# Performance work log

Hardware: AMD Instinct MI355X
Metric: run time of the kernel (lower is better)

## Reference

```python
import jax, jax.numpy as jnp
import numpy as np

N_NODES = 100000
N_EDGES = 3200000
D_NODE = 32
D_EDGE = 6


def _mlp2(x, W1, b1, W2, b2):
    # Linear -> ReLU -> Linear -> ReLU
    h = jax.nn.relu(x @ W1 + b1)
    return jax.nn.relu(h @ W2 + b2)


def setup_inputs() -> dict:
    key = jax.random.key(0)
    ks = jax.random.split(key, 12)
    glorot = lambda k, fi, fo: jax.random.normal(k, (fi, fo), jnp.float32) * (2.0 / (fi + fo)) ** 0.5
    return {
        "x_node": jax.random.normal(ks[0], (N_NODES, D_NODE), jnp.float32),
        "x_edge": jax.random.normal(ks[1], (N_EDGES, D_EDGE), jnp.float32),
        "src": jax.random.randint(ks[2], (N_EDGES,), 0, N_NODES, jnp.int32),
        "dst": jax.random.randint(ks[3], (N_EDGES,), 0, N_NODES, jnp.int32),
        # edge_msg_encoder: 70 -> 32 -> 6
        "We1": glorot(ks[4], 70, 32), "be1": jnp.zeros((32,), jnp.float32),
        "We2": glorot(ks[5], 32, 6), "be2": jnp.zeros((6,), jnp.float32),
        # node_msg_encoder: 38 -> 64 -> 32
        "Wn1": glorot(ks[6], 38, 64), "bn1": jnp.zeros((64,), jnp.float32),
        "Wn2": glorot(ks[7], 64, 32), "bn2": jnp.zeros((32,), jnp.float32),
    }


def reference(x_node, x_edge, src, dst, We1, be1, We2, be2, Wn1, bn1, Wn2, bn2):
    # Gather endpoint node features per edge
    x_dst = x_node[dst]                                   # [E, 32]
    x_src = x_node[src]                                   # [E, 32]
    edge_in = jnp.concatenate([x_dst, x_src, x_edge], 1)  # [E, 70]
    edge_msg = _mlp2(edge_in, We1, be1, We2, be2)         # [E, 6]
    node_in = jnp.concatenate([x_dst, edge_msg], 1)       # [E, 38]
    node_msg = _mlp2(node_in, Wn1, bn1, Wn2, bn2)         # [E, 32]
    # reduce_udf: sum of incoming messages per destination node
    nm = jax.ops.segment_sum(node_msg, dst, num_segments=N_NODES)  # [N, 32]
    return nm, edge_msg
```

## Files before the change

### kernel.cpp

```cpp
#include <hip/hip_runtime.h>

#define N_EDGES 3200000
#define N_NODES 100000

typedef unsigned short ushort_t;
typedef __attribute__((ext_vector_type(8))) short bf16x8;
typedef __attribute__((ext_vector_type(4))) float f32x4;

__device__ inline unsigned short f2bf(float f) {
    unsigned u = __float_as_uint(f);
    u += 0x7fffu + ((u >> 16) & 1u);
    return (unsigned short)(u >> 16);
}
__device__ inline unsigned pack_bf2(float lo, float hi) {
    return (unsigned)f2bf(lo) | ((unsigned)f2bf(hi) << 16);
}
__device__ inline float bflo(unsigned u) { return __uint_as_float(u << 16); }
__device__ inline float bfhi(unsigned u) { return __uint_as_float(u & 0xffff0000u); }
__device__ inline bf16x8 u4_to_b8(uint4 u) {
    union { uint4 a; bf16x8 b; } c; c.a = u; return c.b;
}

__global__ void __launch_bounds__(256) mpn_precompute(
    const float* __restrict__ x_node,
    const float* __restrict__ We1, const float* __restrict__ be1,
    const float* __restrict__ We2, const float* __restrict__ be2,
    const float* __restrict__ Wn1, const float* __restrict__ bn1,
    const float* __restrict__ Wn2,
    unsigned* __restrict__ xb,
    ushort_t* __restrict__ WaT, ushort_t* __restrict__ WbT,
    ushort_t* __restrict__ WcTp, ushort_t* __restrict__ W2T,
    ushort_t* __restrict__ NaT, ushort_t* __restrict__ NbTp,
    ushort_t* __restrict__ N2T, float* __restrict__ be2p,
    float* __restrict__ nm_out)
{
    const int n = blockIdx.x * 256 + threadIdx.x;

    if (n < 1024) {
        const int o = n >> 5, k = n & 31;
        WaT[n] = f2bf(We1[k * 32 + o]);
        WbT[n] = f2bf(We1[(32 + k) * 32 + o]);
        WcTp[n] = (k < 6) ? f2bf(We1[(64 + k) * 32 + o])
                          : ((k == 6) ? f2bf(be1[o]) : (ushort_t)0);
    }
    if (n < 512) {
        const int o = n >> 5, k = n & 31;
        W2T[n] = (o < 6) ? f2bf(We2[k * 6 + o]) : (ushort_t)0;
    }
    if (n < 2048) {
        const int o = n >> 5, k = n & 31;
        NaT[n] = f2bf(Wn1[k * 64 + o]);
        NbTp[n] = (k < 6) ? f2bf(Wn1[(32 + k) * 64 + o])
                          : ((k == 6) ? f2bf(bn1[o]) : (ushort_t)0);
        N2T[n] = f2bf(Wn2[(n & 63) * 32 + (n >> 6)]);
    }
    if (n < 16) be2p[n] = (n < 6) ? be2[n] : 0.0f;

    if (n >= N_NODES) return;

    {
        float4 z = make_float4(0.f, 0.f, 0.f, 0.f);
        float4* o = (float4*)(nm_out + (size_t)n * 32);
        #pragma unroll
        for (int i = 0; i < 8; ++i) o[i] = z;
    }
    {
        const float4* px = (const float4*)(x_node + (size_t)n * 32);
        unsigned* xr = xb + (size_t)n * 16;
        #pragma unroll
        for (int i = 0; i < 8; ++i) {
            float4 v = px[i];
            xr[2*i+0] = pack_bf2(v.x, v.y);
            xr[2*i+1] = pack_bf2(v.z, v.w);
        }
    }
}

__global__ void __launch_bounds__(256, 4) mpn_main(
    const ushort_t* __restrict__ xb,
    const ushort_t* __restrict__ WaT, const ushort_t* __restrict__ WbT,
    const ushort_t* __restrict__ WcTp, const ushort_t* __restrict__ W2T,
    const ushort_t* __restrict__ NaT, const ushort_t* __restrict__ NbTp,
    const ushort_t* __restrict__ N2T,
    const float* __restrict__ be2p, const float* __restrict__ bn2,
    const float* __restrict__ x_edge,
    const int* __restrict__ src, const int* __restrict__ dst,
    float* __restrict__ nm_out,
    float* __restrict__ em_out)
{
    __shared__ unsigned s_nmb[128 * 17];
    __shared__ int s_d[128];

    const int tid  = threadIdx.x;
    const int lane = tid & 63;
    const int wave = tid >> 6;
    const int q    = (lane >> 4) & 3;
    const int l15  = lane & 15;
    const int hi   = q >> 1;

    const int eb = blockIdx.x * 128 + wave * 32;

    int dv[2], sv[2];
    #pragma unroll
    for (int t = 0; t < 2; ++t) {
        const int e = eb + t * 16 + l15;
        dv[t] = dst[e];
        sv[t] = src[e];
    }
    bf16x8 xd[2], xs[2];
    #pragma unroll
    for (int t = 0; t < 2; ++t) {
        xd[t] = *(const bf16x8*)(xb + (size_t)dv[t] * 32 + q * 8);
        xs[t] = *(const bf16x8*)(xb + (size_t)sv[t] * 32 + q * 8);
    }
    uint4 bxeU[2];
    #pragma unroll
    for (int t = 0; t < 2; ++t) {
        uint4 u = make_uint4(0, 0, 0, 0);
        if (q == 0) {
            const int e = eb + t * 16 + l15;
            const float2* pe = (const float2*)(x_edge + (size_t)e * 6);
            float2 a = pe[0], b = pe[1], c = pe[2];
            u = make_uint4(pack_bf2(a.x, a.y), pack_bf2(b.x, b.y),
                           pack_bf2(c.x, c.y), pack_bf2(1.0f, 0.0f));
        }
        bxeU[t] = u;
    }

    const int sAl = ((q & 1) << 5) + l15;
    const int sBl = sAl + 16;

    #pragma unroll
    for (int t = 0; t < 2; ++t) {
        f32x4 h1c[2];
        #pragma unroll
        for (int m = 0; m < 2; ++m) {
            const int row = m * 16 + l15;
            f32x4 acc = (f32x4)0.f;
            acc = __builtin_amdgcn_mfma_f32_16x16x32_bf16(
                *(const bf16x8*)(WaT + row * 32 + q * 8), xd[t], acc, 0, 0, 0);
            acc = __builtin_amdgcn_mfma_f32_16x16x32_bf16(
                *(const bf16x8*)(WbT + row * 32 + q * 8), xs[t], acc, 0, 0, 0);
            acc = __builtin_amdgcn_mfma_f32_16x16x32_bf16(
                *(const bf16x8*)(WcTp + row * 32 + q * 8), u4_to_b8(bxeU[t]), acc, 0, 0, 0);
            #pragma unroll
            for (int r = 0; r < 4; ++r) acc[r] = fmaxf(acc[r], 0.f);
            h1c[m] = acc;
        }

        unsigned u00 = pack_bf2(h1c[0][0], h1c[0][1]);
        unsigned u01 = pack_bf2(h1c[0][2], h1c[0][3]);
        unsigned u10 = pack_bf2(h1c[1][0], h1c[1][1]);
        unsigned u11 = pack_bf2(h1c[1][2], h1c[1][3]);
        unsigned a0 = __shfl((int)u00, sAl), a1 = __shfl((int)u01, sAl);
        unsigned a2 = __shfl((int)u10, sAl), a3 = __shfl((int)u11, sAl);
        unsigned b0 = __shfl((int)u00, sBl), b1 = __shfl((int)u01, sBl);
        unsigned b2 = __shfl((int)u10, sBl), b3 = __shfl((int)u11, sBl);
        uint4 bh1 = make_uint4(hi ? a2 : a0, hi ? a3 : a1,
                               hi ? b2 : b0, hi ? b3 : b1);

        f32x4 emc = __builtin_amdgcn_mfma_f32_16x16x32_bf16(
            *(const bf16x8*)(W2T + l15 * 32 + q * 8), u4_to_b8(bh1),
            (f32x4)0.f, 0, 0, 0);
        const float emv0 = fmaxf(emc[0] + be2p[q * 4 + 0], 0.f);
        const float emv1 = fmaxf(emc[1] + be2p[q * 4 + 1], 0.f);
        const float emv2 = fmaxf(emc[2] + be2p[q * 4 + 2], 0.f);
        const float emv3 = fmaxf(emc[3] + be2p[q * 4 + 3], 0.f);

        const int e = eb + t * 16 + l15;
        if (q == 0) {
            *(float2*)(em_out + (size_t)e * 6 + 0) = make_float2(emv0, emv1);
            *(float2*)(em_out + (size_t)e * 6 + 2) = make_float2(emv2, emv3);
        } else if (q == 1) {
            *(float2*)(em_out + (size_t)e * 6 + 4) = make_float2(emv0, emv1);
        }

        const float f4 = __shfl(emv0, l15 + 16);
        const float f5 = __shfl(emv1, l15 + 16);
        uint4 bem = make_uint4(0, 0, 0, 0);
        if (q == 0)
            bem = make_uint4(pack_bf2(emv0, emv1), pack_bf2(emv2, emv3),
                             pack_bf2(f4, f5), pack_bf2(1.0f, 0.0f));

        f32x4 h2c[4];
        #pragma unroll
        for (int m = 0; m < 4; ++m) {
            const int row = m * 16 + l15;
            f32x4 acc = __builtin_amdgcn_mfma_f32_16x16x32_bf16(
                *(const bf16x8*)(NbTp + row * 32 + q * 8), u4_to_b8(bem),
                (f32x4)0.f, 0, 0, 0);
            acc = __builtin_amdgcn_mfma_f32_16x16x32_bf16(
                *(const bf16x8*)(NaT + row * 32 + q * 8), xd[t], acc, 0, 0, 0);
            #pragma unroll
            for (int r = 0; r < 4; ++r) acc[r] = fmaxf(acc[r], 0.f);
            h2c[m] = acc;
        }

        unsigned v00 = pack_bf2(h2c[0][0], h2c[0][1]), v01 = pack_bf2(h2c[0][2], h2c[0][3]);
        unsigned v10 = pack_bf2(h2c[1][0], h2c[1][1]), v11 = pack_bf2(h2c[1][2], h2c[1][3]);
        unsigned v20 = pack_bf2(h2c[2][0], h2c[2][1]), v21 = pack_bf2(h2c[2][2], h2c[2][3]);
        unsigned v30 = pack_bf2(h2c[3][0], h2c[3][1]), v31 = pack_bf2(h2c[3][2], h2c[3][3]);
        unsigned c0 = __shfl((int)v00, sAl), c1 = __shfl((int)v01, sAl);
        unsigned c2 = __shfl((int)v10, sAl), c3 = __shfl((int)v11, sAl);
        unsigned d0 = __shfl((int)v00, sBl), d1 = __shfl((int)v01, sBl);
        unsigned d2 = __shfl((int)v10, sBl), d3 = __shfl((int)v11, sBl);
        uint4 bh2k0 = make_uint4(hi ? c2 : c0, hi ? c3 : c1,
                                 hi ? d2 : d0, hi ? d3 : d1);
        unsigned g0 = __shfl((int)v20, sAl), g1 = __shfl((int)v21, sAl);
        unsigned g2 = __shfl((int)v30, sAl), g3 = __shfl((int)v31, sAl);
        unsigned k0 = __shfl((int)v20, sBl), k1 = __shfl((int)v21, sBl);
        unsigned k2 = __shfl((int)v30, sBl), k3 = __shfl((int)v31, sBl);
        uint4 bh2k1 = make_uint4(hi ? g2 : g0, hi ? g3 : g1,
                                 hi ? k2 : k0, hi ? k3 : k1);

        f32x4 nm0 = __builtin_amdgcn_mfma_f32_16x16x32_bf16(
            *(const bf16x8*)(N2T + (0 * 16 + l15) * 64 + q * 8), u4_to_b8(bh2k0),
            (f32x4)0.f, 0, 0, 0);
        nm0 = __builtin_amdgcn_mfma_f32_16x16x32_bf16(
            *(const bf16x8*)(N2T + (0 * 16 + l15) * 64 + 32 + q * 8), u4_to_b8(bh2k1),
            nm0, 0, 0, 0);
        f32x4 nm1 = __builtin_amdgcn_mfma_f32_16x16x32_bf16(
            *(const bf16x8*)(N2T + (1 * 16 + l15) * 64 + q * 8), u4_to_b8(bh2k0),
            (f32x4)0.f, 0, 0, 0);
        nm1 = __builtin_amdgcn_mfma_f32_16x16x32_bf16(
            *(const bf16x8*)(N2T + (1 * 16 + l15) * 64 + 32 + q * 8), u4_to_b8(bh2k1),
            nm1, 0, 0, 0);

        #pragma unroll
        for (int r = 0; r < 4; ++r) {
            const int f = q * 4 + r;
            s_nmb[(wave * 32 + t * 16 + l15) * 17 + f] =
                pack_bf2(fmaxf(nm0[r] + bn2[f], 0.f),
                         fmaxf(nm1[r] + bn2[16 + f], 0.f));
        }
        if (q == 0) s_d[wave * 32 + t * 16 + l15] = dv[t];
    }
    __syncthreads();

    #pragma unroll 4
    for (int it = 0; it < 8; ++it) {
        const int idx = it * 256 + tid;
        const int row = idx >> 4;
        const int w   = idx & 15;
        const unsigned u = s_nmb[row * 17 + w];
        float* base = nm_out + (size_t)s_d[row] * 32 + w;
        atomicAdd(base,      bflo(u));
        atomicAdd(base + 16, bfhi(u));
    }
}

extern "C" void kernel_launch(void* const* d_in, const int* in_sizes, int n_in,
                              void* d_out, int out_size, void* d_ws, size_t ws_size,
                              hipStream_t stream) {
    const float* x_node = (const float*)d_in[0];
    const float* x_edge = (const float*)d_in[1];
    const int*   src    = (const int*)d_in[2];
    const int*   dst    = (const int*)d_in[3];
    const float* We1 = (const float*)d_in[4];
    const float* be1 = (const float*)d_in[5];
    const float* We2 = (const float*)d_in[6];
    const float* be2 = (const float*)d_in[7];
    const float* Wn1 = (const float*)d_in[8];
    const float* bn1 = (const float*)d_in[9];
    const float* Wn2 = (const float*)d_in[10];
    const float* bn2 = (const float*)d_in[11];

    float* nm_out = (float*)d_out;
    float* em_out = (float*)d_out + (size_t)N_NODES * 32;

    char* ws = (char*)d_ws;
    unsigned* xb    = (unsigned*)ws;
    ushort_t* WaT   = (ushort_t*)(ws + 6400000);
    ushort_t* WbT   = (ushort_t*)(ws + 6402048);
    ushort_t* WcTp  = (ushort_t*)(ws + 6404096);
    ushort_t* W2T   = (ushort_t*)(ws + 6406144);
    ushort_t* NaT   = (ushort_t*)(ws + 6407168);
    ushort_t* NbTp  = (ushort_t*)(ws + 6411264);
    ushort_t* N2T   = (ushort_t*)(ws + 6415360);
    float*    be2p  = (float*)(ws + 6419456);

    mpn_precompute<<<(N_NODES + 255) / 256, 256, 0, stream>>>(
        x_node, We1, be1, We2, be2, Wn1, bn1, Wn2,
        xb, WaT, WbT, WcTp, W2T, NaT, NbTp, N2T, be2p, nm_out);

    mpn_main<<<N_EDGES / 128, 256, 0, stream>>>(
        (const ushort_t*)xb, WaT, WbT, WcTp, W2T, NaT, NbTp, N2T,
        be2p, bn2, x_edge, src, dst, nm_out, em_out);
}
```

Measured before the change: 551.3 us.

## Pack two fixed-point features per 64-bit integer atomic for scatter-add

```diff
diff --git a/kernel.cpp b/kernel.cpp
--- a/kernel.cpp
+++ b/kernel.cpp
@@ -2,8 +2,11 @@
 
 #define N_EDGES 3200000
 #define N_NODES 100000
+#define SFIX 16384.0f
+#define INVSFIX 6.103515625e-05f
 
 typedef unsigned short ushort_t;
+typedef unsigned long long u64_t;
 typedef __attribute__((ext_vector_type(8))) short bf16x8;
 typedef __attribute__((ext_vector_type(4))) float f32x4;
 
@@ -15,10 +18,13 @@
 __device__ inline unsigned pack_bf2(float lo, float hi) {
     return (unsigned)f2bf(lo) | ((unsigned)f2bf(hi) << 16);
 }
-__device__ inline float bflo(unsigned u) { return __uint_as_float(u << 16); }
-__device__ inline float bfhi(unsigned u) { return __uint_as_float(u & 0xffff0000u); }
 __device__ inline bf16x8 u4_to_b8(uint4 u) {
     union { uint4 a; bf16x8 b; } c; c.a = u; return c.b;
+}
+__device__ inline u64_t fixpair(float lo, float hi) {
+    const unsigned ul = __float2uint_rn(fmaxf(lo, 0.0f) * SFIX);
+    const unsigned uh = __float2uint_rn(fmaxf(hi, 0.0f) * SFIX);
+    return (u64_t)ul | ((u64_t)uh << 32);
 }
 
 __global__ void __launch_bounds__(256) mpn_precompute(
@@ -32,7 +38,7 @@
     ushort_t* __restrict__ WcTp, ushort_t* __restrict__ W2T,
     ushort_t* __restrict__ NaT, ushort_t* __restrict__ NbTp,
     ushort_t* __restrict__ N2T, float* __restrict__ be2p,
-    float* __restrict__ nm_out)
+    u64_t* __restrict__ acc64)
 {
     const int n = blockIdx.x * 256 + threadIdx.x;
 
@@ -59,10 +65,10 @@
     if (n >= N_NODES) return;
 
     {
-        float4 z = make_float4(0.f, 0.f, 0.f, 0.f);
-        float4* o = (float4*)(nm_out + (size_t)n * 32);
+        uint4 z = make_uint4(0, 0, 0, 0);
+        uint4* a = (uint4*)(acc64 + (size_t)n * 16);
         #pragma unroll
-        for (int i = 0; i < 8; ++i) o[i] = z;
+        for (int i = 0; i < 8; ++i) a[i] = z;
     }
     {
         const float4* px = (const float4*)(x_node + (size_t)n * 32);
@@ -85,10 +91,10 @@
     const float* __restrict__ be2p, const float* __restrict__ bn2,
     const float* __restrict__ x_edge,
     const int* __restrict__ src, const int* __restrict__ dst,
-    float* __restrict__ nm_out,
+    u64_t* __restrict__ acc64,
     float* __restrict__ em_out)
 {
-    __shared__ unsigned s_nmb[128 * 17];
+    __shared__ u64_t s_a64[128 * 16];
     __shared__ int s_d[128];
 
     const int tid  = threadIdx.x;
@@ -226,12 +232,14 @@
             *(const bf16x8*)(N2T + (1 * 16 + l15) * 64 + 32 + q * 8), u4_to_b8(bh2k1),
             nm1, 0, 0, 0);
 
-        #pragma unroll
-        for (int r = 0; r < 4; ++r) {
-            const int f = q * 4 + r;
-            s_nmb[(wave * 32 + t * 16 + l15) * 17 + f] =
-                pack_bf2(fmaxf(nm0[r] + bn2[f], 0.f),
-                         fmaxf(nm1[r] + bn2[16 + f], 0.f));
+        {
+            const int row = wave * 32 + t * 16 + l15;
+            u64_t* sr = s_a64 + row * 16;
+            const int f = q * 4;
+            sr[q*2 + 0]     = fixpair(nm0[0] + bn2[f+0], nm0[1] + bn2[f+1]);
+            sr[q*2 + 1]     = fixpair(nm0[2] + bn2[f+2], nm0[3] + bn2[f+3]);
+            sr[8 + q*2 + 0] = fixpair(nm1[0] + bn2[16+f+0], nm1[1] + bn2[16+f+1]);
+            sr[8 + q*2 + 1] = fixpair(nm1[2] + bn2[16+f+2], nm1[3] + bn2[16+f+3]);
         }
         if (q == 0) s_d[wave * 32 + t * 16 + l15] = dv[t];
     }
@@ -241,11 +249,26 @@
     for (int it = 0; it < 8; ++it) {
         const int idx = it * 256 + tid;
         const int row = idx >> 4;
-        const int w   = idx & 15;
-        const unsigned u = s_nmb[row * 17 + w];
-        float* base = nm_out + (size_t)s_d[row] * 32 + w;
-        atomicAdd(base,      bflo(u));
-        atomicAdd(base + 16, bfhi(u));
+        const int j   = idx & 15;
+        atomicAdd(acc64 + (size_t)s_d[row] * 16 + j, s_a64[row * 16 + j]);
+    }
+}
+
+__global__ void __launch_bounds__(256) mpn_convert(
+    const u64_t* __restrict__ acc64,
+    float* __restrict__ nm_out)
+{
+    const int n = blockIdx.x * 256 + threadIdx.x;
+    if (n >= N_NODES) return;
+    const u64_t* a = acc64 + (size_t)n * 16;
+    float4* o = (float4*)(nm_out + (size_t)n * 32);
+    #pragma unroll
+    for (int i = 0; i < 8; ++i) {
+        const u64_t v0 = a[2*i], v1 = a[2*i+1];
+        o[i] = make_float4((float)(unsigned)v0         * INVSFIX,
+                           (float)(unsigned)(v0 >> 32) * INVSFIX,
+                           (float)(unsigned)v1         * INVSFIX,
+                           (float)(unsigned)(v1 >> 32) * INVSFIX);
     }
 }
 
@@ -278,12 +301,15 @@
     ushort_t* NbTp  = (ushort_t*)(ws + 6411264);
     ushort_t* N2T   = (ushort_t*)(ws + 6415360);
     float*    be2p  = (float*)(ws + 6419456);
+    u64_t*    acc64 = (u64_t*)(ws + 6420480);
 
     mpn_precompute<<<(N_NODES + 255) / 256, 256, 0, stream>>>(
         x_node, We1, be1, We2, be2, Wn1, bn1, Wn2,
-        xb, WaT, WbT, WcTp, W2T, NaT, NbTp, N2T, be2p, nm_out);
+        xb, WaT, WbT, WcTp, W2T, NaT, NbTp, N2T, be2p, acc64);
 
     mpn_main<<<N_EDGES / 128, 256, 0, stream>>>(
         (const ushort_t*)xb, WaT, WbT, WcTp, W2T, NaT, NbTp, N2T,
-        be2p, bn2, x_edge, src, dst, nm_out, em_out);
-}
+        be2p, bn2, x_edge, src, dst, acc64, em_out);
+
+    mpn_convert<<<(N_NODES + 255) / 256, 256, 0, stream>>>(acc64, nm_out);
+}
```

Result: slower. 566.4 us (+2.7%).
